# Performance work log

Hardware: AMD Instinct MI355X
Metric: run time of the kernel (lower is better)

The kernel has to match this reference:

```python
import jax, jax.numpy as jnp
import numpy as np

B, N, IN_DIM, H, L = 8, 1024, 3, 256, 3
NUM_STEPS = 200
LN_EPS = 1e-5


def _cdist(a, b):
    # Euclidean pairwise distance, a:[B,n,d], b:[B,m,d] -> [B,n,m]
    d2 = (jnp.sum(a * a, -1)[:, :, None] + jnp.sum(b * b, -1)[:, None, :]
          - 2.0 * jnp.einsum('bik,bjk->bij', a, b))
    d2 = jnp.maximum(d2, 0.0)
    safe = jnp.sqrt(jnp.where(d2 > 0, d2, 1.0))
    return jnp.where(d2 > 0, safe, 0.0)


def _layernorm(x, g, b):
    mu = jnp.mean(x, -1, keepdims=True)
    var = jnp.mean(jnp.square(x - mu), -1, keepdims=True)
    return (x - mu) * jax.lax.rsqrt(var + LN_EPS) * g + b


def setup_inputs() -> dict:
    key = jax.random.key(0)
    ks = jax.random.split(key, 32)
    s = 0.02
    inp = {
        'x': jax.random.normal(ks[0], (B, N, IN_DIM), jnp.float32),
        't': jax.random.randint(ks[1], (B,), 0, NUM_STEPS),
        'mask': jnp.ones((B, N), bool),
        # top-level weights (stored [in,out])
        'w_time': jax.random.normal(ks[2], (1, H)) * s,
        'b_time': jnp.zeros((H,)),
        'w_in': jax.random.normal(ks[3], (IN_DIM + H, H)) * s,
        'b_in': jnp.zeros((H,)),
        'w_out': jax.random.normal(ks[4], (H, IN_DIM)) * s,
        'b_out': jnp.zeros((IN_DIM,)),
        # per-layer stacked params [L, ...]
        'qkv_w': jax.random.normal(ks[5], (L, H, 3 * H)) * s,
        'qkv_b': jnp.zeros((L, 3 * H)),
        'ao_w': jax.random.normal(ks[6], (L, H, H)) * s,
        'ao_b': jnp.zeros((L, H)),
        'fc1_w': jax.random.normal(ks[7], (L, H, 4 * H)) * s,
        'fc1_b': jax.random.normal(ks[8], (L, 4 * H)) * s,
        'fc2_w': jax.random.normal(ks[9], (L, 4 * H, H)) * s,
        'fc2_b': jax.random.normal(ks[10], (L, H)) * s,
        'ln1_g': jnp.ones((L, H)), 'ln1_b': jnp.zeros((L, H)),
        'ln2_g': jnp.ones((L, H)), 'ln2_b': jnp.zeros((L, H)),
    }
    return inp


def reference(x, t, mask, w_time, b_time, w_in, b_in, w_out, b_out,
              qkv_w, qkv_b, ao_w, ao_b, fc1_w, fc1_b, fc2_w, fc2_b,
              ln1_g, ln1_b, ln2_g, ln2_b):
    tf = t.astype(jnp.float32)[:, None] / float(NUM_STEPS)          # [B,1]
    t_embed = jax.nn.relu(tf @ w_time + b_time)                      # [B,H]
    t_embed = jnp.broadcast_to(t_embed[:, None, :], (B, N, H))
    h = jax.nn.relu(jnp.concatenate([x, t_embed], -1) @ w_in + b_in)  # [B,N,H]
    geo = _cdist(h[:, :, :3], h[:, :, :3])                           # [B,N,N]
    mask_f = mask.astype(h.dtype)
    scale = 1.0 / jnp.sqrt(jnp.float32(H))
    for l in range(L):
        qkv = (h @ qkv_w[l] + qkv_b[l]).reshape(B, N, 3, H)
        q, k, v = qkv[:, :, 0], qkv[:, :, 1], qkv[:, :, 2]
        dist = _cdist(geo, geo)                                      # cdist of the distance matrix itself
        scores = jnp.einsum('bik,bjk->bij', q, k) * scale * jnp.exp(-dist)
        scores = jnp.where(mask[:, None, :], scores, -jnp.inf)
        attn = jax.nn.softmax(scores, axis=-1)
        ao = (jnp.einsum('bij,bjk->bik', attn, v) @ ao_w[l] + ao_b[l]) * mask_f[:, :, None]
        xx = _layernorm(h + ao, ln1_g[l], ln1_b[l])
        f1 = jax.nn.relu((xx @ fc1_w[l] + fc1_b[l]) * mask_f[:, :, None])
        ffn = jax.nn.relu((f1 @ fc2_w[l] + fc2_b[l]) * mask_f[:, :, None])
        h = _layernorm(xx + ffn, ln2_g[l], ln2_b[l])
    return (h @ w_out + b_out) * mask_f[:, :, None]
```

## Files before the change

kernel.cpp:

```cpp
#include <hip/hip_runtime.h>
#include <math.h>

#define NB 8
#define NN 1024
#define NH 256
#define NL 3

typedef unsigned short u16;
typedef __bf16 bf16x8 __attribute__((ext_vector_type(8)));
typedef _Float16 f16x8 __attribute__((ext_vector_type(8)));
typedef float f32x4 __attribute__((ext_vector_type(4)));

constexpr int EPI_BIAS_RELU = 2, EPI_EDIST = 5, EPI_QKV = 6;

__device__ __forceinline__ unsigned bf16rne(float f) {
    unsigned u = __float_as_uint(f);
    return (u + 0x7fffu + ((u >> 16) & 1u)) >> 16;
}
__device__ __forceinline__ unsigned bfpair(float a, float b) {
    return bf16rne(a) | (bf16rne(b) << 16);
}
__device__ __forceinline__ float bf2f(u16 h) {
    unsigned u = ((unsigned)h) << 16;
    return __uint_as_float(u);
}

__device__ __forceinline__ float blockSum256(float v) {
    __shared__ float sm[4];
    #pragma unroll
    for (int o = 32; o; o >>= 1) v += __shfl_down(v, o, 64);
    int lane = threadIdx.x & 63, wid = threadIdx.x >> 6;
    if (lane == 0) sm[wid] = v;
    __syncthreads();
    if (threadIdx.x == 0) sm[0] = sm[0] + sm[1] + sm[2] + sm[3];
    __syncthreads();
    float r = sm[0];
    __syncthreads();
    return r;
}

template <int EPI, int DT, bool OBF, int SWZ, int MT>
__global__ __launch_bounds__(256) void gemm_mfma(
    const u16* __restrict__ A, int lda, long sA,
    const u16* __restrict__ Bt, int ldb, long sB,
    void* __restrict__ C, int ldc, long sC,
    int K,
    const float* __restrict__ bias, long sBias,
    u16* __restrict__ vtout)
{
    constexpr int MF = MT / 32;
    constexpr int ASZ = MT * 8;
    __shared__ uint4 sm4[ASZ + 1024];
    const int tid = threadIdx.x;

    int bx = blockIdx.x, by = blockIdx.y, bz = blockIdx.z;
    bool trans = false;
    if (SWZ == 2) {
        int gx = gridDim.x;
        int T = gx * gridDim.y;
        int lid = bx + gx * by;
        int nl = (lid & 7) * (T >> 3) + (lid >> 3);
        bx = nl % gx; by = nl / gx;
    } else if (SWZ == 3) {
        int lid = bx + gridDim.x * bz;
        bz = lid & 7;
        int idx = lid >> 3;
        int j = 0;
        while (idx >= 16 - 2 * j) { idx -= 16 - 2 * j; j++; }
        by = 2 * j + idx;
        bx = j;
        trans = (by >= 2 * bx + 2);
    }
    const int z = bz;
    const int row0 = by * MT, col0 = bx * 128;

    f32x4 acc[MF][4];
    #pragma unroll
    for (int m = 0; m < MF; m++)
        #pragma unroll
        for (int n = 0; n < 4; n++) acc[m][n] = (f32x4){0.f, 0.f, 0.f, 0.f};

    const int l = tid & 63, wid = tid >> 6;
    const int wr = wid >> 1, wc = wid & 1;
    const int lrow = l & 15, lgrp = l >> 4;

    for (int k0 = 0; k0 < K; k0 += 64) {
        if (MT == 128) {
            const int srow = tid >> 1, half = tid & 1, cb = half * 4, swz = srow & 7;
            const u16* Ap = A + (long)z * sA + (long)(row0 + srow) * lda + k0 + half * 32;
            uint4 a0 = *(const uint4*)(Ap + 0),  a1 = *(const uint4*)(Ap + 8);
            uint4 a2 = *(const uint4*)(Ap + 16), a3 = *(const uint4*)(Ap + 24);
            sm4[srow * 8 + ((cb + 0) ^ swz)] = a0;
            sm4[srow * 8 + ((cb + 1) ^ swz)] = a1;
            sm4[srow * 8 + ((cb + 2) ^ swz)] = a2;
            sm4[srow * 8 + ((cb + 3) ^ swz)] = a3;
        } else {
            const int arow = tid >> 2, aq = tid & 3, swz = arow & 7;
            const u16* Ap = A + (long)z * sA + (long)(row0 + arow) * lda + k0 + aq * 16;
            uint4 a0 = *(const uint4*)(Ap + 0), a1 = *(const uint4*)(Ap + 8);
            sm4[arow * 8 + ((aq * 2 + 0) ^ swz)] = a0;
            sm4[arow * 8 + ((aq * 2 + 1) ^ swz)] = a1;
        }
        {
            const int brow = tid >> 1, bq = tid & 1, cb = bq * 4, swz = brow & 7;
            const u16* Bp = Bt + (long)z * sB + (long)(col0 + brow) * ldb + k0 + bq * 32;
            uint4 b0 = *(const uint4*)(Bp + 0),  b1 = *(const uint4*)(Bp + 8);
            uint4 b2 = *(const uint4*)(Bp + 16), b3 = *(const uint4*)(Bp + 24);
            sm4[ASZ + brow * 8 + ((cb + 0) ^ swz)] = b0;
            sm4[ASZ + brow * 8 + ((cb + 1) ^ swz)] = b1;
            sm4[ASZ + brow * 8 + ((cb + 2) ^ swz)] = b2;
            sm4[ASZ + brow * 8 + ((cb + 3) ^ swz)] = b3;
        }
        __syncthreads();

        #pragma unroll
        for (int ks = 0; ks < 2; ks++) {
            int c = ks * 4 + lgrp;
            uint4 a[MF], b[4];
            #pragma unroll
            for (int m = 0; m < MF; m++) {
                int r = wr * (MT / 2) + m * 16 + lrow;
                a[m] = sm4[r * 8 + (c ^ (r & 7))];
            }
            #pragma unroll
            for (int n = 0; n < 4; n++) {
                int r = wc * 64 + n * 16 + lrow;
                b[n] = sm4[ASZ + r * 8 + (c ^ (r & 7))];
            }
            #pragma unroll
            for (int m = 0; m < MF; m++)
                #pragma unroll
                for (int n = 0; n < 4; n++) {
                    if (DT == 0)
                        acc[m][n] = __builtin_amdgcn_mfma_f32_16x16x32_bf16(
                            __builtin_bit_cast(bf16x8, a[m]), __builtin_bit_cast(bf16x8, b[n]), acc[m][n], 0, 0, 0);
                    else
                        acc[m][n] = __builtin_amdgcn_mfma_f32_16x16x32_f16(
                            __builtin_bit_cast(f16x8, a[m]), __builtin_bit_cast(f16x8, b[n]), acc[m][n], 0, 0, 0);
                }
        }
        __syncthreads();
    }

    u16* Ts = (u16*)sm4;
    #pragma unroll
    for (int m = 0; m < MF; m++) {
        #pragma unroll
        for (int n = 0; n < 4; n++) {
            int rbase = row0 + wr * (MT / 2) + m * 16 + lgrp * 4;
            int cc = col0 + wc * 64 + n * 16 + lrow;
            float bv = 0.f;
            if (EPI == EPI_QKV || EPI == EPI_BIAS_RELU)
                bv = bias[cc];
            float vals[4];
            #pragma unroll
            for (int reg = 0; reg < 4; reg++) {
                long r = rbase + reg;
                float v = acc[m][n][reg];
                if (EPI == EPI_QKV) v += bv;
                else if (EPI == EPI_BIAS_RELU) v = fmaxf(v + bv, 0.f);
                else if (EPI == EPI_EDIST) {
                    const float* rnb = bias + (long)z * sBias;
                    float d2 = fmaxf(rnb[r] + rnb[cc] - 2.f * v, 0.f);
                    v = (r == cc) ? 1.f : expf(-sqrtf(d2));
                }
                vals[reg] = v;
                if (OBF) ((u16*)C)[(long)z * sC + r * ldc + cc] = (u16)bf16rne(v);
                else     ((float*)C)[(long)z * sC + r * ldc + cc] = v;
            }
            if (EPI == EPI_EDIST && SWZ == 3 && trans) {
                int cl = cc - col0, rl = rbase - row0;
                uint2 tv;
                tv.x = bfpair(vals[0], vals[1]);
                tv.y = bfpair(vals[2], vals[3]);
                *(uint2*)(Ts + cl * 68 + rl) = tv;
            }
            if (EPI == EPI_QKV && cc >= 512) {
                int b = rbase >> 10;
                uint2 tv;
                tv.x = bfpair(vals[0], vals[1]);
                tv.y = bfpair(vals[2], vals[3]);
                *(uint2*)&vtout[(long)b * NH * NN + (long)(cc - 512) * NN + (rbase & 1023)] = tv;
            }
        }
    }
    if (EPI == EPI_EDIST && SWZ == 3 && trans) {
        __syncthreads();
        int row = tid >> 1, half = tid & 1;
        const u16* src = Ts + row * 68 + half * 32;
        uint2 v0 = *(const uint2*)(src + 0),  v1 = *(const uint2*)(src + 4);
        uint2 v2 = *(const uint2*)(src + 8),  v3 = *(const uint2*)(src + 12);
        uint2 v4 = *(const uint2*)(src + 16), v5 = *(const uint2*)(src + 20);
        uint2 v6 = *(const uint2*)(src + 24), v7 = *(const uint2*)(src + 28);
        uint4* dst = (uint4*)((u16*)C + (long)z * sC + (long)(col0 + row) * ldc + row0 + half * 32);
        uint4 w0 = {v0.x, v0.y, v1.x, v1.y};
        uint4 w1 = {v2.x, v2.y, v3.x, v3.y};
        uint4 w2 = {v4.x, v4.y, v5.x, v5.y};
        uint4 w3 = {v6.x, v6.y, v7.x, v7.y};
        dst[0] = w0; dst[1] = w1; dst[2] = w2; dst[3] = w3;
    }
}

__global__ __launch_bounds__(512) void flash_k(
    const u16* __restrict__ qkv,
    const u16* __restrict__ vt,
    const u16* __restrict__ edist,
    const u16* __restrict__ aow,
    const float* __restrict__ aob,
    const float* __restrict__ hres,
    const float* __restrict__ g1,
    const float* __restrict__ b1,
    float* __restrict__ xb,
    u16* __restrict__ xbbf,
    float scale)
{
    __shared__ __align__(16) u16 Es[32][136];
    __shared__ __align__(16) u16 Ps[32][136];
    __shared__ __align__(16) u16 Os[32 * 264];
    __shared__ float rs[32][8];
    __shared__ float lnA[32][8];
    __shared__ float lnB[32][8];

    const int tid = threadIdx.x;
    const int l = tid & 63, w = tid >> 6;
    const int g = l >> 4, lr = l & 15;

    int lid = blockIdx.x + gridDim.x * blockIdx.y;
    const int b = lid & 7;
    const int q0 = (lid >> 3) * 32;

    const u16* qkvb = qkv + (long)b * NN * 768;
    const u16* vtb  = vt + (long)b * NH * NN;
    const u16* eb   = edist + (long)b * NN * NN;

    uint4 qf[2][8];
    #pragma unroll
    for (int m = 0; m < 2; m++)
        #pragma unroll
        for (int ks = 0; ks < 8; ks++)
            qf[m][ks] = *(const uint4*)(qkvb + (long)(q0 + 16 * m + lr) * 768 + 32 * ks + 8 * g);

    f32x4 oacc[2][2];
    #pragma unroll
    for (int m = 0; m < 2; m++)
        #pragma unroll
        for (int nf = 0; nf < 2; nf++) oacc[m][nf] = (f32x4){0.f, 0.f, 0.f, 0.f};
    float rsum[2][4] = {{0.f, 0.f, 0.f, 0.f}, {0.f, 0.f, 0.f, 0.f}};

    for (int n0 = 0; n0 < NN; n0 += 128) {
        {
            int r = tid >> 4, ch = tid & 15;
            *(uint4*)&Es[r][ch * 8] = *(const uint4*)(eb + (long)(q0 + r) * NN + n0 + ch * 8);
        }
        __syncthreads();

        f32x4 s[2];
        s[0] = (f32x4){0.f, 0.f, 0.f, 0.f};
        s[1] = (f32x4){0.f, 0.f, 0.f, 0.f};
        const u16* kbase = qkvb + (long)(n0 + w * 16 + lr) * 768 + 256;
        #pragma unroll
        for (int ks = 0; ks < 8; ks++) {
            bf16x8 kf = __builtin_bit_cast(bf16x8, *(const uint4*)(kbase + 32 * ks + 8 * g));
            s[0] = __builtin_amdgcn_mfma_f32_16x16x32_bf16(__builtin_bit_cast(bf16x8, qf[0][ks]), kf, s[0], 0, 0, 0);
            s[1] = __builtin_amdgcn_mfma_f32_16x16x32_bf16(__builtin_bit_cast(bf16x8, qf[1][ks]), kf, s[1], 0, 0, 0);
        }
        #pragma unroll
        for (int m = 0; m < 2; m++)
            #pragma unroll
            for (int reg = 0; reg < 4; reg++) {
                int q = 16 * m + 4 * g + reg;
                int kc = w * 16 + lr;
                float p = expf(s[m][reg] * scale * bf2f(Es[q][kc]));
                rsum[m][reg] += p;
                Ps[q][kc] = (u16)bf16rne(p);
            }
        __syncthreads();

        #pragma unroll
        for (int ks = 0; ks < 4; ks++) {
            bf16x8 pa[2], vbf[2];
            #pragma unroll
            for (int m = 0; m < 2; m++)
                pa[m] = __builtin_bit_cast(bf16x8, *(const uint4*)&Ps[16 * m + lr][32 * ks + 8 * g]);
            #pragma unroll
            for (int nf = 0; nf < 2; nf++) {
                int c = w * 32 + nf * 16 + lr;
                vbf[nf] = __builtin_bit_cast(bf16x8, *(const uint4*)(vtb + (long)c * NN + n0 + 32 * ks + 8 * g));
            }
            #pragma unroll
            for (int m = 0; m < 2; m++)
                #pragma unroll
                for (int nf = 0; nf < 2; nf++)
                    oacc[m][nf] = __builtin_amdgcn_mfma_f32_16x16x32_bf16(pa[m], vbf[nf], oacc[m][nf], 0, 0, 0);
        }
    }

    #pragma unroll
    for (int m = 0; m < 2; m++)
        #pragma unroll
        for (int reg = 0; reg < 4; reg++) {
            float v = rsum[m][reg];
            v += __shfl_xor(v, 1); v += __shfl_xor(v, 2);
            v += __shfl_xor(v, 4); v += __shfl_xor(v, 8);
            rsum[m][reg] = v;
        }
    if (lr == 0) {
        #pragma unroll
        for (int m = 0; m < 2; m++)
            #pragma unroll
            for (int reg = 0; reg < 4; reg++)
                rs[16 * m + 4 * g + reg][w] = rsum[m][reg];
    }
    __syncthreads();

    #pragma unroll
    for (int m = 0; m < 2; m++)
        #pragma unroll
        for (int reg = 0; reg < 4; reg++) {
            int q = 16 * m + 4 * g + reg;
            float t = 0.f;
            #pragma unroll
            for (int j = 0; j < 8; j++) t += rs[q][j];
            float inv = 1.f / t;
            #pragma unroll
            for (int nf = 0; nf < 2; nf++) {
                int c = w * 32 + nf * 16 + lr;
                Os[q * 264 + c] = (u16)bf16rne(oacc[m][nf][reg] * inv);
            }
        }
    __syncthreads();

    f32x4 aacc[2][2];
    #pragma unroll
    for (int m = 0; m < 2; m++)
        #pragma unroll
        for (int nf = 0; nf < 2; nf++) aacc[m][nf] = (f32x4){0.f, 0.f, 0.f, 0.f};
    #pragma unroll
    for (int kc = 0; kc < 8; kc++) {
        bf16x8 pa[2], wb[2];
        #pragma unroll
        for (int m = 0; m < 2; m++)
            pa[m] = __builtin_bit_cast(bf16x8, *(const uint4*)&Os[(16 * m + lr) * 264 + kc * 32 + 8 * g]);
        #pragma unroll
        for (int nf = 0; nf < 2; nf++)
            wb[nf] = __builtin_bit_cast(bf16x8, *(const uint4*)(aow + (long)(32 * w + 16 * nf + lr) * 256 + kc * 32 + 8 * g));
        #pragma unroll
        for (int m = 0; m < 2; m++)
            #pragma unroll
            for (int nf = 0; nf < 2; nf++)
                aacc[m][nf] = __builtin_amdgcn_mfma_f32_16x16x32_bf16(pa[m], wb[nf], aacc[m][nf], 0, 0, 0);
    }

    int j0 = 32 * w + lr, j1 = 32 * w + 16 + lr;
    float aob0 = aob[j0], aob1 = aob[j1];
    float xv[2][2][4];
    #pragma unroll
    for (int m = 0; m < 2; m++)
        #pragma unroll
        for (int reg = 0; reg < 4; reg++) {
            int q = 16 * m + 4 * g + reg;
            long hr = ((long)b * NN + q0 + q) * NH;
            xv[m][0][reg] = aacc[m][0][reg] + aob0 + hres[hr + j0];
            xv[m][1][reg] = aacc[m][1][reg] + aob1 + hres[hr + j1];
        }

    #pragma unroll
    for (int m = 0; m < 2; m++)
        #pragma unroll
        for (int reg = 0; reg < 4; reg++) {
            float s = xv[m][0][reg] + xv[m][1][reg];
            float s2 = xv[m][0][reg] * xv[m][0][reg] + xv[m][1][reg] * xv[m][1][reg];
            s  += __shfl_xor(s, 1);  s  += __shfl_xor(s, 2);  s  += __shfl_xor(s, 4);  s  += __shfl_xor(s, 8);
            s2 += __shfl_xor(s2, 1); s2 += __shfl_xor(s2, 2); s2 += __shfl_xor(s2, 4); s2 += __shfl_xor(s2, 8);
            if (lr == 0) {
                int q = 16 * m + 4 * g + reg;
                lnA[q][w] = s;
                lnB[q][w] = s2;
            }
        }
    __syncthreads();

    float g1v0 = g1[j0], g1v1 = g1[j1], b1v0 = b1[j0], b1v1 = b1[j1];
    #pragma unroll
    for (int m = 0; m < 2; m++)
        #pragma unroll
        for (int reg = 0; reg < 4; reg++) {
            int q = 16 * m + 4 * g + reg;
            float S = 0.f, S2 = 0.f;
            #pragma unroll
            for (int j = 0; j < 8; j++) { S += lnA[q][j]; S2 += lnB[q][j]; }
            float mu = S * (1.f / NH);
            float var = S2 * (1.f / NH) - mu * mu;
            float rsd = rsqrtf(var + 1e-5f);
            long hr = ((long)b * NN + q0 + q) * NH;
            float o0 = (xv[m][0][reg] - mu) * rsd * g1v0 + b1v0;
            float o1 = (xv[m][1][reg] - mu) * rsd * g1v1 + b1v1;
            xb[hr + j0] = o0;
            xb[hr + j1] = o1;
            xbbf[hr + j0] = (u16)bf16rne(o0);
            xbbf[hr + j1] = (u16)bf16rne(o1);
        }
}

__global__ __launch_bounds__(256) void fc2ln_k(
    const u16* __restrict__ f1,
    const float* __restrict__ resid,
    const u16* __restrict__ w2,
    const float* __restrict__ b2,
    const float* __restrict__ g2,
    const float* __restrict__ bb2,
    float* __restrict__ hout,
    u16* __restrict__ hbf)
{
    __shared__ uint4 As[256];
    __shared__ uint4 Bs[2048];
    __shared__ float lnA[32][4], lnB[32][4];

    const int tid = threadIdx.x;
    const int l = tid & 63, w = tid >> 6;
    const int lrow = l & 15, lgrp = l >> 4;
    const long r0 = (long)blockIdx.x * 32;

    f32x4 acc[2][4];
    #pragma unroll
    for (int m = 0; m < 2; m++)
        #pragma unroll
        for (int n = 0; n < 4; n++) acc[m][n] = (f32x4){0.f, 0.f, 0.f, 0.f};

    for (int k0 = 0; k0 < 1024; k0 += 64) {
        {
            int row = tid >> 3, ch = tid & 7;
            As[row * 8 + (ch ^ (row & 7))] = *(const uint4*)(f1 + (r0 + row) * 1024 + k0 + ch * 8);
        }
        #pragma unroll
        for (int i = 0; i < 8; i++) {
            int idx = tid + 256 * i;
            int row = idx >> 3, ch = idx & 7;
            Bs[row * 8 + (ch ^ (row & 7))] = *(const uint4*)(w2 + (long)row * 1024 + k0 + ch * 8);
        }
        __syncthreads();
        #pragma unroll
        for (int ks = 0; ks < 2; ks++) {
            int c = ks * 4 + lgrp;
            uint4 a[2], b[4];
            #pragma unroll
            for (int m = 0; m < 2; m++) {
                int r = m * 16 + lrow;
                a[m] = As[r * 8 + (c ^ (r & 7))];
            }
            #pragma unroll
            for (int n = 0; n < 4; n++) {
                int r = 64 * w + n * 16 + lrow;
                b[n] = Bs[r * 8 + (c ^ (r & 7))];
            }
            #pragma unroll
            for (int m = 0; m < 2; m++)
                #pragma unroll
                for (int n = 0; n < 4; n++)
                    acc[m][n] = __builtin_amdgcn_mfma_f32_16x16x32_bf16(
                        __builtin_bit_cast(bf16x8, a[m]), __builtin_bit_cast(bf16x8, b[n]), acc[m][n], 0, 0, 0);
        }
        __syncthreads();
    }

    float xv[2][4][4];
    #pragma unroll
    for (int m = 0; m < 2; m++)
        #pragma unroll
        for (int n = 0; n < 4; n++) {
            int cc = 64 * w + 16 * n + lrow;
            float bv = b2[cc];
            #pragma unroll
            for (int reg = 0; reg < 4; reg++) {
                int rr = 16 * m + 4 * lgrp + reg;
                xv[m][n][reg] = fmaxf(acc[m][n][reg] + bv, 0.f) + resid[(r0 + rr) * 256 + cc];
            }
        }

    #pragma unroll
    for (int m = 0; m < 2; m++)
        #pragma unroll
        for (int reg = 0; reg < 4; reg++) {
            float s = 0.f, s2 = 0.f;
            #pragma unroll
            for (int n = 0; n < 4; n++) {
                s += xv[m][n][reg];
                s2 += xv[m][n][reg] * xv[m][n][reg];
            }
            s  += __shfl_xor(s, 1);  s  += __shfl_xor(s, 2);  s  += __shfl_xor(s, 4);  s  += __shfl_xor(s, 8);
            s2 += __shfl_xor(s2, 1); s2 += __shfl_xor(s2, 2); s2 += __shfl_xor(s2, 4); s2 += __shfl_xor(s2, 8);
            if (lrow == 0) {
                int rr = 16 * m + 4 * lgrp + reg;
                lnA[rr][w] = s;
                lnB[rr][w] = s2;
            }
        }
    __syncthreads();

    #pragma unroll
    for (int m = 0; m < 2; m++)
        #pragma unroll
        for (int reg = 0; reg < 4; reg++) {
            int rr = 16 * m + 4 * lgrp + reg;
            float S = lnA[rr][0] + lnA[rr][1] + lnA[rr][2] + lnA[rr][3];
            float S2 = lnB[rr][0] + lnB[rr][1] + lnB[rr][2] + lnB[rr][3];
            float mu = S * (1.f / NH);
            float var = S2 * (1.f / NH) - mu * mu;
            float rsd = rsqrtf(var + 1e-5f);
            #pragma unroll
            for (int n = 0; n < 4; n++) {
                int cc = 64 * w + 16 * n + lrow;
                float o = (xv[m][n][reg] - mu) * rsd * g2[cc] + bb2[cc];
                hout[(r0 + rr) * 256 + cc] = o;
                hbf[(r0 + rr) * 256 + cc] = (u16)bf16rne(o);
            }
        }
}

__global__ __launch_bounds__(256) void base_k(const int* __restrict__ t,
                                              const float* __restrict__ w_time,
                                              const float* __restrict__ b_time,
                                              const float* __restrict__ w_in,
                                              const float* __restrict__ b_in,
                                              float* __restrict__ base) {
    int b = blockIdx.x, j = threadIdx.x;
    __shared__ float te[256];
    float tf = (float)t[b] / 200.0f;
    te[j] = fmaxf(tf * w_time[j] + b_time[j], 0.f);
    __syncthreads();
    float acc = b_in[j];
    for (int k = 0; k < 256; k++) acc = fmaf(te[k], w_in[(3 + k) * 256 + j], acc);
    base[b * 256 + j] = acc;
}

__global__ __launch_bounds__(256) void hinit_k(const float* __restrict__ x,
                                               const float* __restrict__ w_in,
                                               const float* __restrict__ base,
                                               float* __restrict__ h,
                                               u16* __restrict__ hbf,
                                               float* __restrict__ h3) {
    long row = blockIdx.x;
    int b = (int)(row >> 10);
    int j = threadIdx.x;
    float x0 = x[row * 3 + 0], x1 = x[row * 3 + 1], x2 = x[row * 3 + 2];
    float v = base[b * 256 + j];
    v = fmaf(x0, w_in[j], v);
    v = fmaf(x1, w_in[256 + j], v);
    v = fmaf(x2, w_in[512 + j], v);
    v = fmaxf(v, 0.f);
    h[row * 256 + j] = v;
    hbf[row * 256 + j] = (u16)bf16rne(v);
    if (j < 3) h3[row * 3 + j] = v;
}

__global__ __launch_bounds__(256) void geo_k(const float* __restrict__ h3,
                                             u16* __restrict__ gf,
                                             float* __restrict__ rn) {
    int bi = blockIdx.x;
    int b = bi >> 10, i = bi & 1023;
    const float* hb = h3 + (long)b * NN * 3;
    float ax = hb[i * 3 + 0], ay = hb[i * 3 + 1], az = hb[i * 3 + 2];
    u16* grow = gf + (long)bi * 1024;
    float accs = 0.f;
    #pragma unroll
    for (int j0 = 0; j0 < NN; j0 += 256) {
        int j = j0 + threadIdx.x;
        float dx = hb[j * 3 + 0] - ax, dy = hb[j * 3 + 1] - ay, dz = hb[j * 3 + 2] - az;
        float d2 = dx * dx + dy * dy + dz * dz;
        float d = (d2 > 0.f) ? sqrtf(d2) : 0.f;
        _Float16 hf = (_Float16)d;
        float rep = (float)hf;
        grow[j] = __builtin_bit_cast(u16, hf);
        accs += rep * rep;
    }
    float tot = blockSum256(accs);
    if (threadIdx.x == 0) rn[bi] = tot;
}

__global__ __launch_bounds__(256) void wtrans_k(const float* __restrict__ qkv_w,
                                                const float* __restrict__ ao_w,
                                                const float* __restrict__ fc1_w,
                                                const float* __restrict__ fc2_w,
                                                u16* __restrict__ qkv_wt,
                                                u16* __restrict__ ao_wt,
                                                u16* __restrict__ fc1_wt,
                                                u16* __restrict__ fc2_wt) {
    int type = blockIdx.z, lyr = blockIdx.y;
    int R, Cc;
    const float* src;
    u16* dst;
    if (type == 0) { R = 256; Cc = 768;  src = qkv_w + (long)lyr * R * Cc; dst = qkv_wt + (long)lyr * R * Cc; }
    else if (type == 1) { R = 256; Cc = 256; src = ao_w + (long)lyr * R * Cc; dst = ao_wt + (long)lyr * R * Cc; }
    else if (type == 2) { R = 256; Cc = 1024; src = fc1_w + (long)lyr * R * Cc; dst = fc1_wt + (long)lyr * R * Cc; }
    else { R = 1024; Cc = 256; src = fc2_w + (long)lyr * R * Cc; dst = fc2_wt + (long)lyr * R * Cc; }
    int tC = Cc >> 5, tR = R >> 5;
    int tile = blockIdx.x;
    if (tile >= tC * tR) return;
    int c0 = (tile % tC) << 5, r0 = (tile / tC) << 5;
    __shared__ float tf[32][33];
    int tx = threadIdx.x & 31, ty = threadIdx.x >> 5;
    #pragma unroll
    for (int i = 0; i < 4; i++) {
        int r = ty + 8 * i;
        tf[r][tx] = src[(long)(r0 + r) * Cc + c0 + tx];
    }
    __syncthreads();
    #pragma unroll
    for (int i = 0; i < 4; i++) {
        int c = ty + 8 * i;
        dst[(long)(c0 + c) * R + r0 + tx] = (u16)bf16rne(tf[tx][c]);
    }
}

__global__ __launch_bounds__(256) void out_k(const float* __restrict__ h,
                                             const float* __restrict__ w_out,
                                             const float* __restrict__ b_out,
                                             float* __restrict__ out) {
    long row = blockIdx.x;
    int wid = threadIdx.x >> 6, lane = threadIdx.x & 63;
    if (wid < 3) {
        float acc = 0.f;
        for (int k = lane; k < 256; k += 64) acc = fmaf(h[row * 256 + k], w_out[k * 3 + wid], acc);
        #pragma unroll
        for (int o = 32; o; o >>= 1) acc += __shfl_down(acc, o, 64);
        if (lane == 0) out[row * 3 + wid] = acc + b_out[wid];
    }
}

extern "C" void kernel_launch(void* const* d_in, const int* in_sizes, int n_in,
                              void* d_out, int out_size, void* d_ws, size_t ws_size,
                              hipStream_t stream) {
    const float* x      = (const float*)d_in[0];
    const int*   t      = (const int*)  d_in[1];
    const float* w_time = (const float*)d_in[3];
    const float* b_time = (const float*)d_in[4];
    const float* w_in   = (const float*)d_in[5];
    const float* b_in   = (const float*)d_in[6];
    const float* w_out  = (const float*)d_in[7];
    const float* b_out  = (const float*)d_in[8];
    const float* qkv_w  = (const float*)d_in[9];
    const float* qkv_b  = (const float*)d_in[10];
    const float* ao_w   = (const float*)d_in[11];
    const float* ao_b   = (const float*)d_in[12];
    const float* fc1_w  = (const float*)d_in[13];
    const float* fc1_b  = (const float*)d_in[14];
    const float* fc2_w  = (const float*)d_in[15];
    const float* fc2_b  = (const float*)d_in[16];
    const float* ln1_g  = (const float*)d_in[17];
    const float* ln1_b  = (const float*)d_in[18];
    const float* ln2_g  = (const float*)d_in[19];
    const float* ln2_b  = (const float*)d_in[20];
    float* out = (float*)d_out;

    char* W = (char*)d_ws;
    float* h     = (float*)(W);
    float* xb    = (float*)(W + (8ul << 20));
    u16*   hbf   = (u16*)  (W + (16ul << 20));
    u16*   xbbf  = (u16*)  (W + (20ul << 20));
    u16*   vt    = (u16*)  (W + (24ul << 20));
    u16*   f1    = (u16*)  (W + (28ul << 20));
    u16*   qkvb  = (u16*)  (W + (44ul << 20));
    u16*   edist = (u16*)  (W + (56ul << 20));
    u16*   gf    = (u16*)  (W + (72ul << 20));
    u16*   wts   = (u16*)  (W + (88ul << 20));
    u16* qkv_wt = wts;
    u16* ao_wt  = wts + 589824;
    u16* fc1_wt = wts + 786432;
    u16* fc2_wt = wts + 1572864;
    float* base = (float*)(W + (94ul << 20));
    float* rn   = base + 2048;
    float* h3   = rn + 8192;

    const float scale = 1.0f / 16.0f;

    base_k<<<NB, 256, 0, stream>>>(t, w_time, b_time, w_in, b_in, base);
    hinit_k<<<NB * NN, 256, 0, stream>>>(x, w_in, base, h, hbf, h3);
    geo_k<<<NB * NN, 256, 0, stream>>>(h3, gf, rn);
    wtrans_k<<<dim3(256, NL, 4), 256, 0, stream>>>(qkv_w, ao_w, fc1_w, fc2_w,
                                                   qkv_wt, ao_wt, fc1_wt, fc2_wt);
    gemm_mfma<EPI_EDIST, 1, true, 3, 64><<<dim3(72, 1, 8), 256, 0, stream>>>(
        gf, 1024, (long)NN * 1024, gf, 1024, (long)NN * 1024,
        edist, NN, (long)NN * NN, 1024, rn, NN, nullptr);

    for (int l = 0; l < NL; ++l) {
        gemm_mfma<EPI_QKV, 0, true, 2, 64><<<dim3(6, 128, 1), 256, 0, stream>>>(
            hbf, NH, 0, qkv_wt + (long)l * 196608, NH, 0, qkvb, 768, 0,
            NH, qkv_b + l * 768, 0, vt);
        flash_k<<<dim3(32, 8), 512, 0, stream>>>(
            qkvb, vt, edist, ao_wt + (long)l * 65536, ao_b + l * NH,
            h, ln1_g + l * NH, ln1_b + l * NH, xb, xbbf, scale);
        gemm_mfma<EPI_BIAS_RELU, 0, true, 2, 128><<<dim3(8, 64, 1), 256, 0, stream>>>(
            xbbf, NH, 0, fc1_wt + (long)l * 262144, NH, 0, f1, 1024, 0,
            NH, fc1_b + l * 1024, 0, nullptr);
        fc2ln_k<<<256, 256, 0, stream>>>(
            f1, xb, fc2_wt + (long)l * 262144, fc2_b + l * NH,
            ln2_g + l * NH, ln2_b + l * NH, h, hbf);
    }
    out_k<<<NB * NN, 256, 0, stream>>>(h, w_out, b_out, out);
}
```

Baseline: 360.3 us.

## Software-pipeline K, V and edist tile loads in attention kernel

The attention kernel now prefetches the next tile's K fragments, V fragments and edist row chunk into registers while the current tile's MFMAs run. This replaces the load-then-compute pattern inside each 128-key iteration and is meant to hide global memory latency behind matrix math. The cost is higher register pressure (16 extra uint4 per thread), which may lower occupancy. The last iteration issues a harmless reload of tile 0.

```diff
diff --git a/kernel.cpp b/kernel.cpp
--- a/kernel.cpp
+++ b/kernel.cpp
@@ -240,6 +240,19 @@
         for (int ks = 0; ks < 8; ks++)
             qf[m][ks] = *(const uint4*)(qkvb + (long)(q0 + 16 * m + lr) * 768 + 32 * ks + 8 * g);
 
+    const int er = tid & 31, ech = tid >> 5;
+    const u16* kbase = qkvb + (long)(w * 16 + lr) * 768 + 256;
+    uint4 eC = *(const uint4*)(eb + (long)(q0 + er) * NN + ech * 8);
+    uint4 kf[8], vf[8];
+    #pragma unroll
+    for (int ks = 0; ks < 8; ks++)
+        kf[ks] = *(const uint4*)(kbase + 32 * ks + 8 * g);
+    #pragma unroll
+    for (int ks = 0; ks < 4; ks++)
+        #pragma unroll
+        for (int nf = 0; nf < 2; nf++)
+            vf[ks * 2 + nf] = *(const uint4*)(vtb + (long)(w * 32 + nf * 16 + lr) * NN + 32 * ks + 8 * g);
+
     f32x4 oacc[2][2];
     #pragma unroll
     for (int m = 0; m < 2; m++)
@@ -247,23 +260,26 @@
         for (int nf = 0; nf < 2; nf++) oacc[m][nf] = (f32x4){0.f, 0.f, 0.f, 0.f};
     float rsum[2][4] = {{0.f, 0.f, 0.f, 0.f}, {0.f, 0.f, 0.f, 0.f}};
 
-    for (int n0 = 0; n0 < NN; n0 += 128) {
-        {
-            int r = tid >> 4, ch = tid & 15;
-            *(uint4*)&Es[r][ch * 8] = *(const uint4*)(eb + (long)(q0 + r) * NN + n0 + ch * 8);
-        }
+    for (int it = 0; it < 8; ++it) {
+        const int n1 = (it < 7) ? (it + 1) * 128 : 0;
+
+        *(uint4*)&Es[er][ech * 8] = eC;
         __syncthreads();
 
         f32x4 s[2];
         s[0] = (f32x4){0.f, 0.f, 0.f, 0.f};
         s[1] = (f32x4){0.f, 0.f, 0.f, 0.f};
-        const u16* kbase = qkvb + (long)(n0 + w * 16 + lr) * 768 + 256;
         #pragma unroll
         for (int ks = 0; ks < 8; ks++) {
-            bf16x8 kf = __builtin_bit_cast(bf16x8, *(const uint4*)(kbase + 32 * ks + 8 * g));
-            s[0] = __builtin_amdgcn_mfma_f32_16x16x32_bf16(__builtin_bit_cast(bf16x8, qf[0][ks]), kf, s[0], 0, 0, 0);
-            s[1] = __builtin_amdgcn_mfma_f32_16x16x32_bf16(__builtin_bit_cast(bf16x8, qf[1][ks]), kf, s[1], 0, 0, 0);
-        }
+            bf16x8 kfr = __builtin_bit_cast(bf16x8, kf[ks]);
+            s[0] = __builtin_amdgcn_mfma_f32_16x16x32_bf16(__builtin_bit_cast(bf16x8, qf[0][ks]), kfr, s[0], 0, 0, 0);
+            s[1] = __builtin_amdgcn_mfma_f32_16x16x32_bf16(__builtin_bit_cast(bf16x8, qf[1][ks]), kfr, s[1], 0, 0, 0);
+        }
+        eC = *(const uint4*)(eb + (long)(q0 + er) * NN + n1 + ech * 8);
+        #pragma unroll
+        for (int ks = 0; ks < 8; ks++)
+            kf[ks] = *(const uint4*)(kbase + (long)n1 * 768 + 32 * ks + 8 * g);
+
         #pragma unroll
         for (int m = 0; m < 2; m++)
             #pragma unroll
@@ -278,21 +294,23 @@
 
         #pragma unroll
         for (int ks = 0; ks < 4; ks++) {
-            bf16x8 pa[2], vbf[2];
+            bf16x8 pa[2];
             #pragma unroll
             for (int m = 0; m < 2; m++)
                 pa[m] = __builtin_bit_cast(bf16x8, *(const uint4*)&Ps[16 * m + lr][32 * ks + 8 * g]);
             #pragma unroll
             for (int nf = 0; nf < 2; nf++) {
-                int c = w * 32 + nf * 16 + lr;
-                vbf[nf] = __builtin_bit_cast(bf16x8, *(const uint4*)(vtb + (long)c * NN + n0 + 32 * ks + 8 * g));
-            }
-            #pragma unroll
-            for (int m = 0; m < 2; m++)
+                bf16x8 vbf = __builtin_bit_cast(bf16x8, vf[ks * 2 + nf]);
                 #pragma unroll
-                for (int nf = 0; nf < 2; nf++)
-                    oacc[m][nf] = __builtin_amdgcn_mfma_f32_16x16x32_bf16(pa[m], vbf[nf], oacc[m][nf], 0, 0, 0);
-        }
+                for (int m = 0; m < 2; m++)
+                    oacc[m][nf] = __builtin_amdgcn_mfma_f32_16x16x32_bf16(pa[m], vbf, oacc[m][nf], 0, 0, 0);
+            }
+        }
+        #pragma unroll
+        for (int ks = 0; ks < 4; ks++)
+            #pragma unroll
+            for (int nf = 0; nf < 2; nf++)
+                vf[ks * 2 + nf] = *(const uint4*)(vtb + (long)(w * 32 + nf * 16 + lr) * NN + n1 + 32 * ks + 8 * g);
     }
 
     #pragma unroll
```

New measurement: 338.4 us. 1.06x faster.

## Split attention over key halves and stage K/V tiles in swizzled LDS

Applied to the files above, without the earlier changes.

The fused attention kernel becomes two kernels. A partial kernel handles half of the keys per block, doubling the grid to 512 blocks, and stages K and V^T tiles in XOR-swizzled shared memory instead of reading them straight from global memory. A combine kernel then sums the two fp32 partial outputs and row sums, normalizes, and runs the output projection plus LayerNorm. This adds an extra launch and an fp32 partial-output round trip through memory in exchange for more parallelism and better operand reuse.

```diff
diff --git a/kernel.cpp b/kernel.cpp
--- a/kernel.cpp
+++ b/kernel.cpp
@@ -201,23 +201,150 @@
     }
 }
 
-__global__ __launch_bounds__(512) void flash_k(
+__global__ __launch_bounds__(512) void flash_part_k(
     const u16* __restrict__ qkv,
     const u16* __restrict__ vt,
     const u16* __restrict__ edist,
+    float* __restrict__ po,
+    float* __restrict__ prs,
+    float scale)
+{
+    __shared__ uint4 Ks[64][32];
+    __shared__ uint4 Vts[256][8];
+    __shared__ __align__(16) u16 Es[32][72];
+    __shared__ __align__(16) u16 Ps[32][72];
+    __shared__ float rs[32][4];
+
+    const int tid = threadIdx.x;
+    const int l = tid & 63, w = tid >> 6;
+    const int g = l >> 4, lr = l & 15;
+
+    int lid = blockIdx.x + gridDim.x * blockIdx.y;
+    const int b = lid & 7;
+    const int q0 = (lid >> 3) * 32;
+    const int kh = blockIdx.z;
+    const int kv0 = kh * 512;
+
+    const u16* qkvb = qkv + (long)b * NN * 768;
+    const u16* vtb  = vt + (long)b * NH * NN;
+    const u16* eb   = edist + (long)b * NN * NN;
+
+    const int qm = w >> 2, kf = w & 3;
+
+    uint4 qf[8];
+    #pragma unroll
+    for (int ks = 0; ks < 8; ks++)
+        qf[ks] = *(const uint4*)(qkvb + (long)(q0 + 16 * qm + lr) * 768 + 32 * ks + 8 * g);
+
+    f32x4 oacc[2][2];
+    #pragma unroll
+    for (int m = 0; m < 2; m++)
+        #pragma unroll
+        for (int nf = 0; nf < 2; nf++) oacc[m][nf] = (f32x4){0.f, 0.f, 0.f, 0.f};
+    float rsum[4] = {0.f, 0.f, 0.f, 0.f};
+
+    for (int it = 0; it < 8; ++it) {
+        const int n0 = kv0 + it * 64;
+        #pragma unroll
+        for (int i = 0; i < 4; i++) {
+            int idx = tid + 512 * i;
+            int row = idx >> 5, ch = idx & 31;
+            Ks[row][ch ^ (row & 7)] = *(const uint4*)(qkvb + (long)(n0 + row) * 768 + 256 + ch * 8);
+        }
+        #pragma unroll
+        for (int i = 0; i < 4; i++) {
+            int idx = tid + 512 * i;
+            int c = idx >> 3, ch = idx & 7;
+            Vts[c][ch ^ (c & 7)] = *(const uint4*)(vtb + (long)c * NN + n0 + ch * 8);
+        }
+        if (tid < 256) {
+            int r = tid >> 3, ch = tid & 7;
+            *(uint4*)&Es[r][ch * 8] = *(const uint4*)(eb + (long)(q0 + r) * NN + n0 + ch * 8);
+        }
+        __syncthreads();
+
+        f32x4 s = (f32x4){0.f, 0.f, 0.f, 0.f};
+        const int krow = 16 * kf + lr;
+        #pragma unroll
+        for (int ks = 0; ks < 8; ks++) {
+            bf16x8 kfrag = __builtin_bit_cast(bf16x8, Ks[krow][(4 * ks + g) ^ (krow & 7)]);
+            s = __builtin_amdgcn_mfma_f32_16x16x32_bf16(__builtin_bit_cast(bf16x8, qf[ks]), kfrag, s, 0, 0, 0);
+        }
+        #pragma unroll
+        for (int reg = 0; reg < 4; reg++) {
+            int q = 16 * qm + 4 * g + reg;
+            int kc = 16 * kf + lr;
+            float p = expf(s[reg] * scale * bf2f(Es[q][kc]));
+            rsum[reg] += p;
+            Ps[q][kc] = (u16)bf16rne(p);
+        }
+        __syncthreads();
+
+        #pragma unroll
+        for (int ks = 0; ks < 2; ks++) {
+            bf16x8 pa[2];
+            #pragma unroll
+            for (int m = 0; m < 2; m++)
+                pa[m] = __builtin_bit_cast(bf16x8, *(const uint4*)&Ps[16 * m + lr][32 * ks + 8 * g]);
+            #pragma unroll
+            for (int nf = 0; nf < 2; nf++) {
+                int c = 32 * w + 16 * nf + lr;
+                bf16x8 vbf = __builtin_bit_cast(bf16x8, Vts[c][(4 * ks + g) ^ (c & 7)]);
+                #pragma unroll
+                for (int m = 0; m < 2; m++)
+                    oacc[m][nf] = __builtin_amdgcn_mfma_f32_16x16x32_bf16(pa[m], vbf, oacc[m][nf], 0, 0, 0);
+            }
+        }
+        __syncthreads();
+    }
+
+    #pragma unroll
+    for (int reg = 0; reg < 4; reg++) {
+        float v = rsum[reg];
+        v += __shfl_xor(v, 1); v += __shfl_xor(v, 2);
+        v += __shfl_xor(v, 4); v += __shfl_xor(v, 8);
+        rsum[reg] = v;
+    }
+    if (lr == 0) {
+        #pragma unroll
+        for (int reg = 0; reg < 4; reg++)
+            rs[16 * qm + 4 * g + reg][kf] = rsum[reg];
+    }
+    __syncthreads();
+
+    const long pbase = ((long)(kh * 8 + b) * NN + q0) * NH;
+    #pragma unroll
+    for (int m = 0; m < 2; m++)
+        #pragma unroll
+        for (int nf = 0; nf < 2; nf++)
+            #pragma unroll
+            for (int reg = 0; reg < 4; reg++) {
+                int q = 16 * m + 4 * g + reg;
+                int c = 32 * w + 16 * nf + lr;
+                po[pbase + (long)q * NH + c] = oacc[m][nf][reg];
+            }
+    if ((w & 3) == 0 && lr == 0) {
+        #pragma unroll
+        for (int reg = 0; reg < 4; reg++) {
+            int q = 16 * (w >> 2) + 4 * g + reg;
+            float tot = rs[q][0] + rs[q][1] + rs[q][2] + rs[q][3];
+            prs[(long)kh * 8192 + b * 1024 + q0 + q] = tot;
+        }
+    }
+}
+
+__global__ __launch_bounds__(512) void combine_k(
+    const float* __restrict__ po,
+    const float* __restrict__ prs,
     const u16* __restrict__ aow,
     const float* __restrict__ aob,
     const float* __restrict__ hres,
     const float* __restrict__ g1,
     const float* __restrict__ b1,
     float* __restrict__ xb,
-    u16* __restrict__ xbbf,
-    float scale)
+    u16* __restrict__ xbbf)
 {
-    __shared__ __align__(16) u16 Es[32][136];
-    __shared__ __align__(16) u16 Ps[32][136];
     __shared__ __align__(16) u16 Os[32 * 264];
-    __shared__ float rs[32][8];
     __shared__ float lnA[32][8];
     __shared__ float lnB[32][8];
 
@@ -229,105 +356,29 @@
     const int b = lid & 7;
     const int q0 = (lid >> 3) * 32;
 
-    const u16* qkvb = qkv + (long)b * NN * 768;
-    const u16* vtb  = vt + (long)b * NH * NN;
-    const u16* eb   = edist + (long)b * NN * NN;
-
-    uint4 qf[2][8];
-    #pragma unroll
-    for (int m = 0; m < 2; m++)
-        #pragma unroll
-        for (int ks = 0; ks < 8; ks++)
-            qf[m][ks] = *(const uint4*)(qkvb + (long)(q0 + 16 * m + lr) * 768 + 32 * ks + 8 * g);
-
-    f32x4 oacc[2][2];
-    #pragma unroll
-    for (int m = 0; m < 2; m++)
-        #pragma unroll
-        for (int nf = 0; nf < 2; nf++) oacc[m][nf] = (f32x4){0.f, 0.f, 0.f, 0.f};
-    float rsum[2][4] = {{0.f, 0.f, 0.f, 0.f}, {0.f, 0.f, 0.f, 0.f}};
-
-    for (int n0 = 0; n0 < NN; n0 += 128) {
-        {
-            int r = tid >> 4, ch = tid & 15;
-            *(uint4*)&Es[r][ch * 8] = *(const uint4*)(eb + (long)(q0 + r) * NN + n0 + ch * 8);
-        }
-        __syncthreads();
-
-        f32x4 s[2];
-        s[0] = (f32x4){0.f, 0.f, 0.f, 0.f};
-        s[1] = (f32x4){0.f, 0.f, 0.f, 0.f};
-        const u16* kbase = qkvb + (long)(n0 + w * 16 + lr) * 768 + 256;
-        #pragma unroll
-        for (int ks = 0; ks < 8; ks++) {
-            bf16x8 kf = __builtin_bit_cast(bf16x8, *(const uint4*)(kbase + 32 * ks + 8 * g));
-            s[0] = __builtin_amdgcn_mfma_f32_16x16x32_bf16(__builtin_bit_cast(bf16x8, qf[0][ks]), kf, s[0], 0, 0, 0);
-            s[1] = __builtin_amdgcn_mfma_f32_16x16x32_bf16(__builtin_bit_cast(bf16x8, qf[1][ks]), kf, s[1], 0, 0, 0);
-        }
-        #pragma unroll
-        for (int m = 0; m < 2; m++)
+    const long HALF = (long)8 * NN * NH;
+
+    #pragma unroll
+    for (int m = 0; m < 2; m++) {
+        float inv[4];
+        #pragma unroll
+        for (int reg = 0; reg < 4; reg++) {
+            int q = 16 * m + 4 * g + reg;
+            float t = prs[b * 1024 + q0 + q] + prs[8192 + b * 1024 + q0 + q];
+            inv[reg] = 1.f / t;
+        }
+        #pragma unroll
+        for (int nf = 0; nf < 2; nf++) {
+            int c = 32 * w + 16 * nf + lr;
             #pragma unroll
             for (int reg = 0; reg < 4; reg++) {
                 int q = 16 * m + 4 * g + reg;
-                int kc = w * 16 + lr;
-                float p = expf(s[m][reg] * scale * bf2f(Es[q][kc]));
-                rsum[m][reg] += p;
-                Ps[q][kc] = (u16)bf16rne(p);
-            }
-        __syncthreads();
-
-        #pragma unroll
-        for (int ks = 0; ks < 4; ks++) {
-            bf16x8 pa[2], vbf[2];
-            #pragma unroll
-            for (int m = 0; m < 2; m++)
-                pa[m] = __builtin_bit_cast(bf16x8, *(const uint4*)&Ps[16 * m + lr][32 * ks + 8 * g]);
-            #pragma unroll
-            for (int nf = 0; nf < 2; nf++) {
-                int c = w * 32 + nf * 16 + lr;
-                vbf[nf] = __builtin_bit_cast(bf16x8, *(const uint4*)(vtb + (long)c * NN + n0 + 32 * ks + 8 * g));
-            }
-            #pragma unroll
-            for (int m = 0; m < 2; m++)
-                #pragma unroll
-                for (int nf = 0; nf < 2; nf++)
-                    oacc[m][nf] = __builtin_amdgcn_mfma_f32_16x16x32_bf16(pa[m], vbf[nf], oacc[m][nf], 0, 0, 0);
-        }
-    }
-
-    #pragma unroll
-    for (int m = 0; m < 2; m++)
-        #pragma unroll
-        for (int reg = 0; reg < 4; reg++) {
-            float v = rsum[m][reg];
-            v += __shfl_xor(v, 1); v += __shfl_xor(v, 2);
-            v += __shfl_xor(v, 4); v += __shfl_xor(v, 8);
-            rsum[m][reg] = v;
-        }
-    if (lr == 0) {
-        #pragma unroll
-        for (int m = 0; m < 2; m++)
-            #pragma unroll
-            for (int reg = 0; reg < 4; reg++)
-                rs[16 * m + 4 * g + reg][w] = rsum[m][reg];
-    }
-    __syncthreads();
-
-    #pragma unroll
-    for (int m = 0; m < 2; m++)
-        #pragma unroll
-        for (int reg = 0; reg < 4; reg++) {
-            int q = 16 * m + 4 * g + reg;
-            float t = 0.f;
-            #pragma unroll
-            for (int j = 0; j < 8; j++) t += rs[q][j];
-            float inv = 1.f / t;
-            #pragma unroll
-            for (int nf = 0; nf < 2; nf++) {
-                int c = w * 32 + nf * 16 + lr;
-                Os[q * 264 + c] = (u16)bf16rne(oacc[m][nf][reg] * inv);
-            }
-        }
+                long i0 = ((long)b * NN + q0 + q) * NH + c;
+                float o = (po[i0] + po[HALF + i0]) * inv[reg];
+                Os[q * 264 + c] = (u16)bf16rne(o);
+            }
+        }
+    }
     __syncthreads();
 
     f32x4 aacc[2][2];
@@ -670,6 +721,8 @@
     float* base = (float*)(W + (94ul << 20));
     float* rn   = base + 2048;
     float* h3   = rn + 8192;
+    float* prs  = (float*)(W + (95ul << 20));
+    float* po   = (float*)(W + (96ul << 20));
 
     const float scale = 1.0f / 16.0f;
 
@@ -686,9 +739,11 @@
         gemm_mfma<EPI_QKV, 0, true, 2, 64><<<dim3(6, 128, 1), 256, 0, stream>>>(
             hbf, NH, 0, qkv_wt + (long)l * 196608, NH, 0, qkvb, 768, 0,
             NH, qkv_b + l * 768, 0, vt);
-        flash_k<<<dim3(32, 8), 512, 0, stream>>>(
-            qkvb, vt, edist, ao_wt + (long)l * 65536, ao_b + l * NH,
-            h, ln1_g + l * NH, ln1_b + l * NH, xb, xbbf, scale);
+        flash_part_k<<<dim3(32, 8, 2), 512, 0, stream>>>(
+            qkvb, vt, edist, po, prs, scale);
+        combine_k<<<dim3(32, 8), 512, 0, stream>>>(
+            po, prs, ao_wt + (long)l * 65536, ao_b + l * NH,
+            h, ln1_g + l * NH, ln1_b + l * NH, xb, xbbf);
         gemm_mfma<EPI_BIAS_RELU, 0, true, 2, 128><<<dim3(8, 64, 1), 256, 0, stream>>>(
             xbbf, NH, 0, fc1_wt + (long)l * 262144, NH, 0, f1, 1024, 0,
             NH, fc1_b + l * 1024, 0, nullptr);
```

Result: no change. 357.0 us (-0.9%).
